# Performance work log

Hardware: AMD Instinct MI355X
Metric: run time of the kernel (lower is better)

Reference implementation:

```python
import jax, jax.numpy as jnp
import numpy as np
from jax import lax

D_MODEL, D_INNER, N_STATE, DT_RANK, K = 1024, 2048, 16, 64, 3
B_SZ, SEQ = 2, 1024

def silu(v):
    return v * jax.nn.sigmoid(v)

def setup_inputs() -> dict:
    key = jax.random.key(0)
    ks = jax.random.split(key, 12)
    s = 0.02
    return {
        'x': jax.random.normal(ks[0], (B_SZ, SEQ, D_MODEL), jnp.float32),
        'A_log': jax.random.normal(ks[1], (D_INNER, N_STATE), jnp.float32) * 0.5,
        'W_in': jax.random.normal(ks[2], (D_MODEL, 2 * D_INNER), jnp.float32) * s,
        'b_in': jax.random.normal(ks[3], (2 * D_INNER,), jnp.float32) * s,
        'conv_w': jax.random.normal(ks[4], (D_INNER, 1, K), jnp.float32) * s,  # depthwise [O,I/g,K]
        'conv_b': jax.random.normal(ks[5], (D_INNER,), jnp.float32) * s,
        'W_x': jax.random.normal(ks[6], (D_INNER, DT_RANK + 2 * N_STATE), jnp.float32) * s,
        'W_dt': jax.random.normal(ks[7], (DT_RANK, D_INNER), jnp.float32) * s,
        'b_dt': jax.random.normal(ks[8], (D_INNER,), jnp.float32) * s,
        'W_out': jax.random.normal(ks[9], (D_INNER, D_MODEL), jnp.float32) * s,
        'b_out': jax.random.normal(ks[10], (D_MODEL,), jnp.float32) * s,
    }

def selective_scan(u, delta, A, B, C):
    # u, delta: [b,l,d]; A: [d,n]; B, C: [b,l,n]
    deltaA = jnp.exp(jnp.einsum('bld,dn->bldn', delta, A))          # [b,l,d,n]
    deltaBu = jnp.einsum('bld,bln,bld->bldn', delta, B, u)           # [b,l,d,n]
    h0 = jnp.zeros((u.shape[0], u.shape[2], A.shape[1]), u.dtype)    # [b,d,n]
    def step(h, inp):
        dA_t, dBu_t, C_t = inp
        h = dA_t * h + dBu_t
        y = jnp.einsum('bdn,bn->bd', h, C_t)
        return h, y
    xs = (jnp.moveaxis(deltaA, 1, 0), jnp.moveaxis(deltaBu, 1, 0), jnp.moveaxis(C, 1, 0))
    _, ys = lax.scan(step, h0, xs)                                   # [l,b,d]
    return jnp.moveaxis(ys, 0, 1)                                    # [b,l,d]

def reference(x, A_log, W_in, b_in, conv_w, conv_b, W_x, W_dt, b_dt, W_out, b_out):
    xr = x @ W_in + b_in                                             # [b,l,2*d_inner]
    u, res = jnp.split(xr, 2, axis=-1)
    # causal depthwise conv1d (pad left k-1, truncate == torch pad=k-1 then slice)
    uc = lax.conv_general_dilated(
        jnp.moveaxis(u, 1, 2), conv_w, window_strides=(1,),
        padding=[(K - 1, 0)], feature_group_count=D_INNER,
        dimension_numbers=('NCH', 'OIH', 'NCH'))
    u = silu(jnp.moveaxis(uc, 2, 1) + conv_b)                        # [b,l,d_inner]
    xp = u @ W_x                                                     # [b,l,dt_rank+2n]
    dt, Bm, Cm = jnp.split(xp, [DT_RANK, DT_RANK + N_STATE], axis=-1)
    delta = jax.nn.softplus(dt @ W_dt + b_dt)                        # [b,l,d_inner]
    A = -jnp.exp(A_log)                                              # [d_inner,n]
    y = selective_scan(u, delta, A, Bm, Cm)                          # [b,l,d_inner]
    y = y * silu(res)
    return y @ W_out + b_out
```

## Files before the change

### kernel.cpp

```cpp
#include <hip/hip_runtime.h>

#define D_MODEL 1024
#define D_INNER 2048
#define N_ST    16
#define DT_RANK 64
#define BSZ     2
#define SEQL    1024
#define NTOK    (BSZ*SEQL)
#define NC      64
#define LC      (SEQL/NC)

typedef __attribute__((ext_vector_type(4))) float f32x4;
typedef __attribute__((ext_vector_type(8))) short bf16x8;

__device__ __forceinline__ short f2b(float f) {
  unsigned u = __builtin_bit_cast(unsigned, f);
  u += 0x7fffu + ((u >> 16) & 1u);
  return (short)(u >> 16);
}

__device__ __forceinline__ float b2f(unsigned short s) {
  return __builtin_bit_cast(float, (unsigned)s << 16);
}

__device__ __forceinline__ void gload16(const void* g, void* l) {
  __builtin_amdgcn_global_load_lds(
      (const __attribute__((address_space(1))) void*)g,
      (__attribute__((address_space(3))) void*)l, 16, 0, 0);
}

template<int SOFTPLUS, int PARTIAL, int RESSPLIT>
__global__ __launch_bounds__(256)
void gemm_kernel(const short* __restrict__ A, const short* __restrict__ Bm,
                 const float* __restrict__ bias, float* __restrict__ C,
                 short* __restrict__ upb, short* __restrict__ resb,
                 int M, int N, int K, int lda, int ldb, int ldc, int kChunk)
{
  __shared__ short sA[2][128 * 64];
  __shared__ short sB[2][128 * 64];
  const int tid  = threadIdx.x;
  const int lane = tid & 63;
  const int wave = tid >> 6;
  const int wr = wave >> 1, wc = wave & 1;
  const int lr = lane & 15, lg = lane >> 4;
  const int m0 = blockIdx.y * 128;
  const int n0 = blockIdx.x * 128;
  const int kStart = blockIdx.z * kChunk;
  int kEnd = kStart + kChunk; if (kEnd > K) kEnd = K;
  const int nt = (kEnd - kStart) >> 6;

  if (PARTIAL) C += (size_t)blockIdx.z * M * ldc;

  const int srow = lane >> 3;
  const int scol = ((lane & 7) ^ srow) * 8;
  const short* aS = A + (size_t)(m0 + wave * 32 + srow) * lda + scol + kStart;
  const short* bS = Bm + (size_t)(n0 + wave * 32 + srow) * ldb + scol + kStart;
  const int ldsOff = wave * 2048;

#define STAGE(buf, koff)                                                   \
  {                                                                        \
    _Pragma("unroll")                                                      \
    for (int i_ = 0; i_ < 4; ++i_) {                                       \
      gload16(aS + (size_t)(i_ * 8) * lda + (koff), &sA[buf][ldsOff + i_ * 512]); \
      gload16(bS + (size_t)(i_ * 8) * ldb + (koff), &sB[buf][ldsOff + i_ * 512]); \
    }                                                                      \
  }

  f32x4 acc[4][4];
#pragma unroll
  for (int i = 0; i < 4; ++i)
#pragma unroll
    for (int j = 0; j < 4; ++j) acc[i][j] = (f32x4){0.f, 0.f, 0.f, 0.f};

  STAGE(0, 0);
  __syncthreads();

  for (int t = 0; t < nt; ++t) {
    const int cur = t & 1;
    if (t + 1 < nt) STAGE(cur ^ 1, (t + 1) * 64);

#pragma unroll
    for (int kk = 0; kk < 2; ++kk) {
      bf16x8 aF[4], bF[4];
#pragma unroll
      for (int mi = 0; mi < 4; ++mi) {
        const int row = wr * 64 + mi * 16 + lr;
        aF[mi] = *reinterpret_cast<const bf16x8*>(
            &sA[cur][row * 64 + (((kk * 4 + lg) ^ (lr & 7)) * 8)]);
      }
#pragma unroll
      for (int ni = 0; ni < 4; ++ni) {
        const int row = wc * 64 + ni * 16 + lr;
        bF[ni] = *reinterpret_cast<const bf16x8*>(
            &sB[cur][row * 64 + (((kk * 4 + lg) ^ (lr & 7)) * 8)]);
      }
#pragma unroll
      for (int mi = 0; mi < 4; ++mi)
#pragma unroll
        for (int ni = 0; ni < 4; ++ni)
          acc[mi][ni] = __builtin_amdgcn_mfma_f32_16x16x32_bf16(
              aF[mi], bF[ni], acc[mi][ni], 0, 0, 0);
    }
    __syncthreads();
  }
#undef STAGE

#pragma unroll
  for (int mi = 0; mi < 4; ++mi) {
    const int row = m0 + wr * 64 + mi * 16 + lg * 4;
#pragma unroll
    for (int ni = 0; ni < 4; ++ni) {
      const int col = n0 + wc * 64 + ni * 16 + lr;
      if (RESSPLIT) {
        const float bv = bias[col];
        if (col < 2048) {
#pragma unroll
          for (int j = 0; j < 4; ++j)
            upb[(size_t)(row + j) * 2048 + col] = f2b(acc[mi][ni][j] + bv);
        } else {
#pragma unroll
          for (int j = 0; j < 4; ++j) {
            float v = acc[mi][ni][j] + bv;
            resb[(size_t)(row + j) * 2048 + (col - 2048)] =
                f2b(v / (1.f + __expf(-v)));
          }
        }
      } else if (col < N) {
        float bv = (bias != nullptr && blockIdx.z == 0) ? bias[col] : 0.f;
#pragma unroll
        for (int j = 0; j < 4; ++j) {
          float v = acc[mi][ni][j] + bv;
          if (SOFTPLUS) v = fmaxf(v, 0.f) + log1pf(__expf(-fabsf(v)));
          C[(size_t)(row + j) * ldc + col] = v;
        }
      }
    }
  }
}

__device__ __forceinline__ void trans_body(const float* __restrict__ in,
                                           short* __restrict__ out,
                                           int R, int C, int bx, int by,
                                           short (*t)[33], int tidx)
{
  const int c0 = bx * 32, r0 = by * 32;
  const int cc = tidx & 31, rr = tidx >> 5;
#pragma unroll
  for (int i = 0; i < 4; ++i)
    t[rr + i * 8][cc] = f2b(in[(size_t)(r0 + rr + i * 8) * C + c0 + cc]);
  __syncthreads();
#pragma unroll
  for (int i = 0; i < 4; ++i)
    out[(size_t)(c0 + rr + i * 8) * R + r0 + cc] = t[cc][rr + i * 8];
}

#define PB_CAST  2048
#define PB_WIN   4096
#define PB_WX    192
#define PB_WDT   128
#define PB_WOUT  2048

__global__ __launch_bounds__(256)
void prep_kernel(const float* __restrict__ x,    const float* __restrict__ W_in,
                 const float* __restrict__ W_x,  const float* __restrict__ W_dt,
                 const float* __restrict__ W_out,
                 short* __restrict__ xb,  short* __restrict__ Wib,
                 short* __restrict__ Wxb, short* __restrict__ Wdtb,
                 short* __restrict__ Wob)
{
  __shared__ short t[32][33];
  const int bid = blockIdx.x, tidx = threadIdx.x;
  if (bid < PB_CAST) {
    const int i = bid * 256 + tidx;
    float4 v = *reinterpret_cast<const float4*>(x + (size_t)i * 4);
    *reinterpret_cast<short4*>(xb + (size_t)i * 4) =
        make_short4(f2b(v.x), f2b(v.y), f2b(v.z), f2b(v.w));
  } else if (bid < PB_CAST + PB_WIN) {
    const int b = bid - PB_CAST;
    trans_body(W_in, Wib, 1024, 4096, b % 128, b / 128, t, tidx);
  } else if (bid < PB_CAST + PB_WIN + PB_WX) {
    const int b = bid - PB_CAST - PB_WIN;
    trans_body(W_x, Wxb, 2048, 96, b % 3, b / 3, t, tidx);
  } else if (bid < PB_CAST + PB_WIN + PB_WX + PB_WDT) {
    const int b = bid - PB_CAST - PB_WIN - PB_WX;
    trans_body(W_dt, Wdtb, 64, 2048, b % 64, b / 64, t, tidx);
  } else {
    const int b = bid - PB_CAST - PB_WIN - PB_WX - PB_WDT;
    trans_body(W_out, Wob, 2048, 1024, b % 32, b / 32, t, tidx);
  }
}

__global__ __launch_bounds__(256)
void combine16_kernel(const float* __restrict__ part, float* __restrict__ xp,
                      short* __restrict__ dtb)
{
  const int gid = blockIdx.x * 256 + threadIdx.x;
  const int r = gid / 24, q = gid - r * 24;
  float4 s = make_float4(0.f, 0.f, 0.f, 0.f);
#pragma unroll
  for (int c = 0; c < 16; ++c) {
    const float4 v = *reinterpret_cast<const float4*>(
        part + (size_t)c * 2048 * 96 + (size_t)r * 96 + q * 4);
    s.x += v.x; s.y += v.y; s.z += v.z; s.w += v.w;
  }
  *reinterpret_cast<float4*>(xp + (size_t)r * 96 + q * 4) = s;
  if (q < 16)
    *reinterpret_cast<short4*>(dtb + (size_t)r * 64 + q * 4) =
        make_short4(f2b(s.x), f2b(s.y), f2b(s.z), f2b(s.w));
}

__global__ __launch_bounds__(256)
void combine4_kernel(const float* __restrict__ part, const float* __restrict__ bias,
                     float* __restrict__ out)
{
  const int gid = blockIdx.x * 256 + threadIdx.x;
  const int r = gid >> 8, c4 = gid & 255;
  const float4 bv = *reinterpret_cast<const float4*>(bias + c4 * 4);
  float4 s = bv;
#pragma unroll
  for (int z = 0; z < 4; ++z) {
    const float4 v = *reinterpret_cast<const float4*>(
        part + (size_t)z * 2048 * 1024 + (size_t)r * 1024 + c4 * 4);
    s.x += v.x; s.y += v.y; s.z += v.z; s.w += v.w;
  }
  *reinterpret_cast<float4*>(out + (size_t)r * 1024 + c4 * 4) = s;
}

__global__ __launch_bounds__(256)
void conv_silu_kernel(const unsigned short* __restrict__ up, const float* __restrict__ cw,
                      const float* __restrict__ cb, short* __restrict__ ub)
{
  int i  = blockIdx.x * 256 + threadIdx.x;
  int t  = i >> 9;
  int dq = (i & 511) << 2;
  int l  = t & (SEQL - 1);
  float4 w0 = *reinterpret_cast<const float4*>(cw + dq * 3);
  float4 w1 = *reinterpret_cast<const float4*>(cw + dq * 3 + 4);
  float4 w2 = *reinterpret_cast<const float4*>(cw + dq * 3 + 8);
  float4 bb = *reinterpret_cast<const float4*>(cb + dq);
  ushort4 X2 = *reinterpret_cast<const ushort4*>(up + (size_t)t * 2048 + dq);
  ushort4 z4; z4.x = z4.y = z4.z = z4.w = 0;
  ushort4 X1 = (l >= 1) ? *reinterpret_cast<const ushort4*>(up + (size_t)(t - 1) * 2048 + dq) : z4;
  ushort4 X0 = (l >= 2) ? *reinterpret_cast<const ushort4*>(up + (size_t)(t - 2) * 2048 + dq) : z4;
  float r0 = bb.x + w0.x * b2f(X0.x) + w0.y * b2f(X1.x) + w0.z * b2f(X2.x);
  float r1 = bb.y + w0.w * b2f(X0.y) + w1.x * b2f(X1.y) + w1.y * b2f(X2.y);
  float r2 = bb.z + w1.z * b2f(X0.z) + w1.w * b2f(X1.z) + w2.x * b2f(X2.z);
  float r3 = bb.w + w2.y * b2f(X0.w) + w2.z * b2f(X1.w) + w2.w * b2f(X2.w);
  float o0 = r0 / (1.f + __expf(-r0));
  float o1 = r1 / (1.f + __expf(-r1));
  float o2 = r2 / (1.f + __expf(-r2));
  float o3 = r3 / (1.f + __expf(-r3));
  *reinterpret_cast<short4*>(ub + (size_t)t * 2048 + dq) =
      make_short4(f2b(o0), f2b(o1), f2b(o2), f2b(o3));
}

__global__ __launch_bounds__(256, 4)
void scan_pass1(const float* __restrict__ delta, const unsigned short* __restrict__ ub,
                const float* __restrict__ xp, const float* __restrict__ A_log,
                float* __restrict__ sdl, float* __restrict__ HS)
{
  const int d = blockIdx.y * 256 + threadIdx.x;
  const int c = blockIdx.x, b = blockIdx.z;
  const int t0 = (b << 10) + c * LC;
  float Ac[16];
#pragma unroll
  for (int q = 0; q < 4; ++q) {
    float4 a = *reinterpret_cast<const float4*>(A_log + (size_t)d * 16 + q * 4);
    Ac[q * 4 + 0] = -__expf(a.x); Ac[q * 4 + 1] = -__expf(a.y);
    Ac[q * 4 + 2] = -__expf(a.z); Ac[q * 4 + 3] = -__expf(a.w);
  }
  float h[16];
#pragma unroll
  for (int n = 0; n < 16; ++n) h[n] = 0.f;
  float sd = 0.f;
  const float* dp = delta + (size_t)t0 * 2048 + d;
  const unsigned short* up = ub + (size_t)t0 * 2048 + d;
  const float* xb = xp + (size_t)t0 * 96 + DT_RANK;
#pragma unroll 4
  for (int t = 0; t < LC; ++t) {
    float dl = dp[(size_t)t * 2048];
    float ul = b2f(up[(size_t)t * 2048]);
    float Bf[16];
#pragma unroll
    for (int q = 0; q < 4; ++q)
      *reinterpret_cast<float4*>(&Bf[q * 4]) =
          *reinterpret_cast<const float4*>(xb + (size_t)t * 96 + q * 4);
    float dlu = dl * ul;
    sd += dl;
#pragma unroll
    for (int n = 0; n < 16; ++n)
      h[n] = __expf(dl * Ac[n]) * h[n] + dlu * Bf[n];
  }
  sdl[((size_t)b * NC + c) * 2048 + d] = sd;
  float* hs = HS + (((size_t)b * NC + c) * 2048 + d) * 16;
#pragma unroll
  for (int q = 0; q < 4; ++q)
    *reinterpret_cast<float4*>(hs + q * 4) =
        make_float4(h[q * 4], h[q * 4 + 1], h[q * 4 + 2], h[q * 4 + 3]);
}

__global__ __launch_bounds__(256)
void scan_pass2(const float* __restrict__ sdl, const float* __restrict__ A_log,
                float* __restrict__ HS)
{
  const int gid = blockIdx.x * 256 + threadIdx.x;
  const int b = gid >> 15, rest = gid & 32767;
  const int d = rest >> 4;
  const float Ac = -__expf(A_log[rest]);
  float h = 0.f;
  for (int c = 0; c < NC; ++c) {
    const size_t idx = (((size_t)b * NC + c) << 15) + rest;
    float S = HS[idx];
    float sd = sdl[((size_t)b * NC + c) * 2048 + d];
    HS[idx] = h;
    h = __expf(sd * Ac) * h + S;
  }
}

__global__ __launch_bounds__(256, 4)
void scan_pass3(const float* __restrict__ delta, const unsigned short* __restrict__ ub,
                const float* __restrict__ xp, const float* __restrict__ A_log,
                const float* __restrict__ HS, const unsigned short* __restrict__ rb,
                short* __restrict__ zb)
{
  const int d = blockIdx.y * 256 + threadIdx.x;
  const int c = blockIdx.x, b = blockIdx.z;
  const int t0 = (b << 10) + c * LC;
  float Ac[16];
#pragma unroll
  for (int q = 0; q < 4; ++q) {
    float4 a = *reinterpret_cast<const float4*>(A_log + (size_t)d * 16 + q * 4);
    Ac[q * 4 + 0] = -__expf(a.x); Ac[q * 4 + 1] = -__expf(a.y);
    Ac[q * 4 + 2] = -__expf(a.z); Ac[q * 4 + 3] = -__expf(a.w);
  }
  float h[16];
  const float* hs = HS + (((size_t)b * NC + c) * 2048 + d) * 16;
#pragma unroll
  for (int q = 0; q < 4; ++q) {
    float4 v = *reinterpret_cast<const float4*>(hs + q * 4);
    h[q * 4 + 0] = v.x; h[q * 4 + 1] = v.y; h[q * 4 + 2] = v.z; h[q * 4 + 3] = v.w;
  }
  const float* dp = delta + (size_t)t0 * 2048 + d;
  const unsigned short* up = ub + (size_t)t0 * 2048 + d;
  const float* xb = xp + (size_t)t0 * 96 + DT_RANK;
  const float* xc = xp + (size_t)t0 * 96 + DT_RANK + N_ST;
  const unsigned short* rp = rb + (size_t)t0 * 2048 + d;
  short* zp = zb + (size_t)t0 * 2048 + d;
#pragma unroll 4
  for (int t = 0; t < LC; ++t) {
    float dl = dp[(size_t)t * 2048];
    float ul = b2f(up[(size_t)t * 2048]);
    float rv = b2f(rp[(size_t)t * 2048]);
    float Bf[16], Cf[16];
#pragma unroll
    for (int q = 0; q < 4; ++q) {
      *reinterpret_cast<float4*>(&Bf[q * 4]) =
          *reinterpret_cast<const float4*>(xb + (size_t)t * 96 + q * 4);
      *reinterpret_cast<float4*>(&Cf[q * 4]) =
          *reinterpret_cast<const float4*>(xc + (size_t)t * 96 + q * 4);
    }
    float dlu = dl * ul;
    float p0 = 0.f, p1 = 0.f, p2 = 0.f, p3 = 0.f;
#pragma unroll
    for (int n = 0; n < 16; ++n) {
      h[n] = __expf(dl * Ac[n]) * h[n] + dlu * Bf[n];
      float t2 = h[n] * Cf[n];
      if ((n & 3) == 0) p0 += t2;
      else if ((n & 3) == 1) p1 += t2;
      else if ((n & 3) == 2) p2 += t2;
      else p3 += t2;
    }
    float p = (p0 + p1) + (p2 + p3);
    zp[(size_t)t * 2048] = f2b(p * rv);
  }
}

extern "C" void kernel_launch(void* const* d_in, const int* in_sizes, int n_in,
                              void* d_out, int out_size, void* d_ws, size_t ws_size,
                              hipStream_t stream)
{
  const float* x      = (const float*)d_in[0];
  const float* A_log  = (const float*)d_in[1];
  const float* W_in   = (const float*)d_in[2];
  const float* b_in   = (const float*)d_in[3];
  const float* conv_w = (const float*)d_in[4];
  const float* conv_b = (const float*)d_in[5];
  const float* W_x    = (const float*)d_in[6];
  const float* W_dt   = (const float*)d_in[7];
  const float* b_dt   = (const float*)d_in[8];
  const float* W_out  = (const float*)d_in[9];
  const float* b_out  = (const float*)d_in[10];
  float* out = (float*)d_out;

  char* p = (char*)d_ws;
  short* upb    = (short*)p; p += (size_t)NTOK * 2048 * 2;
  short* rb     = (short*)p; p += (size_t)NTOK * 2048 * 2;
  short* ub     = (short*)p; p += (size_t)NTOK * 2048 * 2;
  float* xp     = (float*)p; p += (size_t)NTOK * 96 * 4;
  short* dtb    = (short*)p; p += (size_t)NTOK * 64 * 2;
  float* delta  = (float*)p; p += (size_t)NTOK * 2048 * 4;
  short* zb     = (short*)p; p += (size_t)NTOK * 2048 * 2;
  short* xb     = (short*)p; p += (size_t)NTOK * 1024 * 2;
  short* Wib    = (short*)p; p += (size_t)4096 * 1024 * 2;
  short* Wxb    = (short*)p; p += (size_t)128 * 2048 * 2;
  short* Wdtb   = (short*)p; p += (size_t)2048 * 64 * 2;
  short* Wob    = (short*)p; p += (size_t)1024 * 2048 * 2;
  float* scr    = (float*)p; p += (size_t)4 * 2048 * 1024 * 4;
  float* xppart = scr;
  float* opart  = scr;
  float* sdl    = (float*)p; p += (size_t)BSZ * NC * 2048 * 4;
  float* HS     = (float*)p; p += (size_t)BSZ * NC * 2048 * 16 * 4;

  prep_kernel<<<dim3(PB_CAST + PB_WIN + PB_WX + PB_WDT + PB_WOUT), 256, 0, stream>>>(
      x, W_in, W_x, W_dt, W_out, xb, Wib, Wxb, Wdtb, Wob);

  gemm_kernel<0, 0, 1><<<dim3(32, 16, 1), 256, 0, stream>>>(
      xb, Wib, b_in, nullptr, upb, rb, NTOK, 4096, 1024, 1024, 1024, 0, 1024);
  conv_silu_kernel<<<dim3(4096), 256, 0, stream>>>(
      (const unsigned short*)upb, conv_w, conv_b, ub);
  gemm_kernel<0, 1, 0><<<dim3(1, 16, 16), 256, 0, stream>>>(
      ub, Wxb, nullptr, xppart, nullptr, nullptr, NTOK, 96, 2048, 2048, 2048, 96, 128);
  combine16_kernel<<<dim3(192), 256, 0, stream>>>(xppart, xp, dtb);
  gemm_kernel<1, 0, 0><<<dim3(16, 16, 1), 256, 0, stream>>>(
      dtb, Wdtb, b_dt, delta, nullptr, nullptr, NTOK, 2048, 64, 64, 64, 2048, 64);
  scan_pass1<<<dim3(NC, 8, BSZ), 256, 0, stream>>>(
      delta, (const unsigned short*)ub, xp, A_log, sdl, HS);
  scan_pass2<<<dim3(256), 256, 0, stream>>>(sdl, A_log, HS);
  scan_pass3<<<dim3(NC, 8, BSZ), 256, 0, stream>>>(
      delta, (const unsigned short*)ub, xp, A_log, HS, (const unsigned short*)rb, zb);
  gemm_kernel<0, 1, 0><<<dim3(8, 16, 4), 256, 0, stream>>>(
      zb, Wob, nullptr, opart, nullptr, nullptr, NTOK, 1024, 2048, 2048, 2048, 1024, 512);
  combine4_kernel<<<dim3(2048), 256, 0, stream>>>(opart, b_out, out);
}
```

Before: 158.0 us.

## Store delta as bf16, tighten GEMM prefetch waits, batch scan_pass2 loads

The softplus GEMM now writes delta as bf16 instead of fp32, which halves the delta traffic read by both scan passes. The GEMM main loop replaces __syncthreads with explicit vmcnt waits plus raw barriers, so the next tile's loads can stay in flight across the barrier. scan_pass2 preloads all chunk sums and states into registers and computes the exponentials before the serial recurrence. The costs are reduced delta precision feeding an exponential recurrence, and more register pressure in pass2.

```diff
diff --git a/kernel.cpp b/kernel.cpp
--- a/kernel.cpp
+++ b/kernel.cpp
@@ -29,7 +29,7 @@
       (__attribute__((address_space(3))) void*)l, 16, 0, 0);
 }
 
-template<int SOFTPLUS, int PARTIAL, int RESSPLIT>
+template<int SOFTPLUS, int PARTIAL, int RESSPLIT, int OUTB16>
 __global__ __launch_bounds__(256)
 void gemm_kernel(const short* __restrict__ A, const short* __restrict__ Bm,
                  const float* __restrict__ bias, float* __restrict__ C,
@@ -73,11 +73,16 @@
     for (int j = 0; j < 4; ++j) acc[i][j] = (f32x4){0.f, 0.f, 0.f, 0.f};
 
   STAGE(0, 0);
-  __syncthreads();
 
   for (int t = 0; t < nt; ++t) {
     const int cur = t & 1;
-    if (t + 1 < nt) STAGE(cur ^ 1, (t + 1) * 64);
+    if (t + 1 < nt) {
+      STAGE(cur ^ 1, (t + 1) * 64);
+      asm volatile("s_waitcnt vmcnt(8)" ::: "memory");
+    } else {
+      asm volatile("s_waitcnt vmcnt(0)" ::: "memory");
+    }
+    __builtin_amdgcn_s_barrier();
 
 #pragma unroll
     for (int kk = 0; kk < 2; ++kk) {
@@ -101,7 +106,7 @@
           acc[mi][ni] = __builtin_amdgcn_mfma_f32_16x16x32_bf16(
               aF[mi], bF[ni], acc[mi][ni], 0, 0, 0);
     }
-    __syncthreads();
+    __builtin_amdgcn_s_barrier();
   }
 #undef STAGE
 
@@ -124,6 +129,14 @@
             resb[(size_t)(row + j) * 2048 + (col - 2048)] =
                 f2b(v / (1.f + __expf(-v)));
           }
+        }
+      } else if (OUTB16) {
+        const float bv = bias[col];
+#pragma unroll
+        for (int j = 0; j < 4; ++j) {
+          float v = acc[mi][ni][j] + bv;
+          if (SOFTPLUS) v = fmaxf(v, 0.f) + log1pf(__expf(-fabsf(v)));
+          upb[(size_t)(row + j) * ldc + col] = f2b(v);
         }
       } else if (col < N) {
         float bv = (bias != nullptr && blockIdx.z == 0) ? bias[col] : 0.f;
@@ -255,7 +268,7 @@
 }
 
 __global__ __launch_bounds__(256, 4)
-void scan_pass1(const float* __restrict__ delta, const unsigned short* __restrict__ ub,
+void scan_pass1(const unsigned short* __restrict__ deltab, const unsigned short* __restrict__ ub,
                 const float* __restrict__ xp, const float* __restrict__ A_log,
                 float* __restrict__ sdl, float* __restrict__ HS)
 {
@@ -273,12 +286,12 @@
 #pragma unroll
   for (int n = 0; n < 16; ++n) h[n] = 0.f;
   float sd = 0.f;
-  const float* dp = delta + (size_t)t0 * 2048 + d;
+  const unsigned short* dp = deltab + (size_t)t0 * 2048 + d;
   const unsigned short* up = ub + (size_t)t0 * 2048 + d;
   const float* xb = xp + (size_t)t0 * 96 + DT_RANK;
 #pragma unroll 4
   for (int t = 0; t < LC; ++t) {
-    float dl = dp[(size_t)t * 2048];
+    float dl = b2f(dp[(size_t)t * 2048]);
     float ul = b2f(up[(size_t)t * 2048]);
     float Bf[16];
 #pragma unroll
@@ -307,18 +320,26 @@
   const int b = gid >> 15, rest = gid & 32767;
   const int d = rest >> 4;
   const float Ac = -__expf(A_log[rest]);
+  float P[NC], S[NC];
+#pragma unroll
+  for (int c = 0; c < NC; ++c)
+    P[c] = sdl[(((size_t)b * NC + c) << 11) + d];
+#pragma unroll
+  for (int c = 0; c < NC; ++c)
+    S[c] = HS[(((size_t)b * NC + c) << 15) + rest];
+#pragma unroll
+  for (int c = 0; c < NC; ++c)
+    P[c] = __expf(P[c] * Ac);
   float h = 0.f;
+#pragma unroll
   for (int c = 0; c < NC; ++c) {
-    const size_t idx = (((size_t)b * NC + c) << 15) + rest;
-    float S = HS[idx];
-    float sd = sdl[((size_t)b * NC + c) * 2048 + d];
-    HS[idx] = h;
-    h = __expf(sd * Ac) * h + S;
+    HS[(((size_t)b * NC + c) << 15) + rest] = h;
+    h = P[c] * h + S[c];
   }
 }
 
 __global__ __launch_bounds__(256, 4)
-void scan_pass3(const float* __restrict__ delta, const unsigned short* __restrict__ ub,
+void scan_pass3(const unsigned short* __restrict__ deltab, const unsigned short* __restrict__ ub,
                 const float* __restrict__ xp, const float* __restrict__ A_log,
                 const float* __restrict__ HS, const unsigned short* __restrict__ rb,
                 short* __restrict__ zb)
@@ -340,7 +361,7 @@
     float4 v = *reinterpret_cast<const float4*>(hs + q * 4);
     h[q * 4 + 0] = v.x; h[q * 4 + 1] = v.y; h[q * 4 + 2] = v.z; h[q * 4 + 3] = v.w;
   }
-  const float* dp = delta + (size_t)t0 * 2048 + d;
+  const unsigned short* dp = deltab + (size_t)t0 * 2048 + d;
   const unsigned short* up = ub + (size_t)t0 * 2048 + d;
   const float* xb = xp + (size_t)t0 * 96 + DT_RANK;
   const float* xc = xp + (size_t)t0 * 96 + DT_RANK + N_ST;
@@ -348,7 +369,7 @@
   short* zp = zb + (size_t)t0 * 2048 + d;
 #pragma unroll 4
   for (int t = 0; t < LC; ++t) {
-    float dl = dp[(size_t)t * 2048];
+    float dl = b2f(dp[(size_t)t * 2048]);
     float ul = b2f(up[(size_t)t * 2048]);
     float rv = b2f(rp[(size_t)t * 2048]);
     float Bf[16], Cf[16];
@@ -398,7 +419,7 @@
   short* ub     = (short*)p; p += (size_t)NTOK * 2048 * 2;
   float* xp     = (float*)p; p += (size_t)NTOK * 96 * 4;
   short* dtb    = (short*)p; p += (size_t)NTOK * 64 * 2;
-  float* delta  = (float*)p; p += (size_t)NTOK * 2048 * 4;
+  short* deltab = (short*)p; p += (size_t)NTOK * 2048 * 2;
   short* zb     = (short*)p; p += (size_t)NTOK * 2048 * 2;
   short* xb     = (short*)p; p += (size_t)NTOK * 1024 * 2;
   short* Wib    = (short*)p; p += (size_t)4096 * 1024 * 2;
@@ -414,21 +435,22 @@
   prep_kernel<<<dim3(PB_CAST + PB_WIN + PB_WX + PB_WDT + PB_WOUT), 256, 0, stream>>>(
       x, W_in, W_x, W_dt, W_out, xb, Wib, Wxb, Wdtb, Wob);
 
-  gemm_kernel<0, 0, 1><<<dim3(32, 16, 1), 256, 0, stream>>>(
+  gemm_kernel<0, 0, 1, 0><<<dim3(32, 16, 1), 256, 0, stream>>>(
       xb, Wib, b_in, nullptr, upb, rb, NTOK, 4096, 1024, 1024, 1024, 0, 1024);
   conv_silu_kernel<<<dim3(4096), 256, 0, stream>>>(
       (const unsigned short*)upb, conv_w, conv_b, ub);
-  gemm_kernel<0, 1, 0><<<dim3(1, 16, 16), 256, 0, stream>>>(
+  gemm_kernel<0, 1, 0, 0><<<dim3(1, 16, 16), 256, 0, stream>>>(
       ub, Wxb, nullptr, xppart, nullptr, nullptr, NTOK, 96, 2048, 2048, 2048, 96, 128);
   combine16_kernel<<<dim3(192), 256, 0, stream>>>(xppart, xp, dtb);
-  gemm_kernel<1, 0, 0><<<dim3(16, 16, 1), 256, 0, stream>>>(
-      dtb, Wdtb, b_dt, delta, nullptr, nullptr, NTOK, 2048, 64, 64, 64, 2048, 64);
+  gemm_kernel<1, 0, 0, 1><<<dim3(16, 16, 1), 256, 0, stream>>>(
+      dtb, Wdtb, b_dt, nullptr, deltab, nullptr, NTOK, 2048, 64, 64, 64, 2048, 64);
   scan_pass1<<<dim3(NC, 8, BSZ), 256, 0, stream>>>(
-      delta, (const unsigned short*)ub, xp, A_log, sdl, HS);
+      (const unsigned short*)deltab, (const unsigned short*)ub, xp, A_log, sdl, HS);
   scan_pass2<<<dim3(256), 256, 0, stream>>>(sdl, A_log, HS);
   scan_pass3<<<dim3(NC, 8, BSZ), 256, 0, stream>>>(
-      delta, (const unsigned short*)ub, xp, A_log, HS, (const unsigned short*)rb, zb);
-  gemm_kernel<0, 1, 0><<<dim3(8, 16, 4), 256, 0, stream>>>(
+      (const unsigned short*)deltab, (const unsigned short*)ub, xp, A_log, HS,
+      (const unsigned short*)rb, zb);
+  gemm_kernel<0, 1, 0, 0><<<dim3(8, 16, 4), 256, 0, stream>>>(
       zb, Wob, nullptr, opart, nullptr, nullptr, NTOK, 1024, 2048, 2048, 2048, 1024, 512);
   combine4_kernel<<<dim3(2048), 256, 0, stream>>>(opart, b_out, out);
 }
```

After: 151.3 us. -4.2%, faster.
